# Performance work log

Hardware: AMD Instinct MI355X
Metric: run time of the kernel (lower is better)

Reference implementation:

```python
import jax, jax.numpy as jnp
import numpy as np

D_MODEL = 1024
NUM_HEADS = 16
D_K = D_MODEL // NUM_HEADS


def setup_inputs() -> dict:
    key = jax.random.key(0)
    ks = jax.random.split(key, 11)
    B, S = 4, 2048
    s = 1.0 / np.sqrt(D_MODEL)
    return {
        "q": jax.random.normal(ks[0], (B, S, D_MODEL), jnp.float32),
        "k": jax.random.normal(ks[1], (B, S, D_MODEL), jnp.float32),
        "v": jax.random.normal(ks[2], (B, S, D_MODEL), jnp.float32),
        "w_q": jax.random.normal(ks[3], (D_MODEL, D_MODEL), jnp.float32) * s,
        "b_q": jnp.zeros((D_MODEL,), jnp.float32),
        "w_k": jax.random.normal(ks[4], (D_MODEL, D_MODEL), jnp.float32) * s,
        "b_k": jnp.zeros((D_MODEL,), jnp.float32),
        "w_v": jax.random.normal(ks[5], (D_MODEL, D_MODEL), jnp.float32) * s,
        "b_v": jnp.zeros((D_MODEL,), jnp.float32),
        "w_o": jax.random.normal(ks[6], (D_MODEL, D_MODEL), jnp.float32) * s,
        "b_o": jnp.zeros((D_MODEL,), jnp.float32),
    }


def reference(q, k, v, w_q, b_q, w_k, b_k, w_v, b_v, w_o, b_o):
    B, S, _ = q.shape
    # projections; torch Linear computes x @ W.T + b
    def proj(x, w, b):
        y = x @ w.T + b
        return y.reshape(B, -1, NUM_HEADS, D_K).transpose(0, 2, 1, 3)  # (B,H,S,d_k)

    qh, kh, vh = proj(q, w_q, b_q), proj(k, w_k, b_k), proj(v, w_v, b_v)
    scores = jnp.einsum("bhqd,bhkd->bhqk", qh, kh) / jnp.sqrt(jnp.float32(D_K))
    attn_weights = jax.nn.softmax(scores, axis=-1)
    x = jnp.einsum("bhqk,bhkd->bhqd", attn_weights, vh)
    x = x.transpose(0, 2, 1, 3).reshape(B, -1, D_MODEL)
    out = x @ w_o.T + b_o
    return out, attn_weights
```

## Files before the change

### kernel.cpp

```cpp
#include <hip/hip_runtime.h>
#include <math.h>

#define S_LEN 2048
#define DM 1024
#define NH 16
#define DK 64

typedef __attribute__((ext_vector_type(8))) short short8;
typedef __attribute__((ext_vector_type(4))) short short4v;
typedef __attribute__((ext_vector_type(4))) float f32x4;

__device__ __forceinline__ short f2bf(float f) {
  unsigned u = __builtin_bit_cast(unsigned, f);
  u = (u + 0x7FFFu + ((u >> 16) & 1u)) >> 16;
  return (short)u;
}

__device__ __forceinline__ void gld_lds16(const short* g, short* l) {
  __builtin_amdgcn_global_load_lds(
      (const __attribute__((address_space(1))) unsigned int*)g,
      (__attribute__((address_space(3))) unsigned int*)l, 16, 0, 0);
}

__global__ __launch_bounds__(256) void cvt_bf16(
    const float* __restrict__ s0, const float* __restrict__ s1,
    const float* __restrict__ s2, const float* __restrict__ s3,
    short* __restrict__ d0, short* __restrict__ d1,
    short* __restrict__ d2, short* __restrict__ d3, int n)
{
  const float* s; short* d;
  switch (blockIdx.y) {
    case 0:  s = s0; d = d0; break;
    case 1:  s = s1; d = d1; break;
    case 2:  s = s2; d = d2; break;
    default: s = s3; d = d3; break;
  }
  const int i = (blockIdx.x * 256 + threadIdx.x) * 8;
  if (i < n) {
    const float4 v0 = *(const float4*)&s[i];
    const float4 v1 = *(const float4*)&s[i + 4];
    short8 r = { f2bf(v0.x), f2bf(v0.y), f2bf(v0.z), f2bf(v0.w),
                 f2bf(v1.x), f2bf(v1.y), f2bf(v1.z), f2bf(v1.w) };
    *(short8*)&d[i] = r;
  }
}

__global__ __launch_bounds__(256) void proj3(
    const short* __restrict__ qb, const short* __restrict__ kb, const short* __restrict__ vb,
    const short* __restrict__ wqb, const short* __restrict__ wkb, const short* __restrict__ wvb,
    const float* __restrict__ biq, const float* __restrict__ bik, const float* __restrict__ biv,
    short* __restrict__ qhb, short* __restrict__ khb, short* __restrict__ vtb)
{
  __shared__ short As[128 * 32];
  __shared__ short Bs[128 * 32];
  const int z = blockIdx.z;
  const short* A; const short* B; const float* bias; short* o;
  if (z == 0)      { A = qb; B = wqb; bias = biq; o = qhb; }
  else if (z == 1) { A = kb; B = wkb; bias = bik; o = khb; }
  else             { A = vb; B = wvb; bias = biv; o = vtb; }

  const int tid = threadIdx.x;
  const int lane = tid & 63;
  const int wv = tid >> 6;
  const int grp = lane >> 4, lid = lane & 15;
  const int wr = wv >> 1, wc = wv & 1;
  const int bm = blockIdx.x, bn = blockIdx.y;

  f32x4 acc[4][4] = {};

  const int idx0 = tid, idx1 = 256 + tid;
  const int r0 = idx0 >> 2, c0 = (idx0 & 3) * 8;
  const int r1 = idx1 >> 2, c1 = (idx1 & 3) * 8;
  const short* a0 = &A[(size_t)(bm * 128 + r0) * DM + c0];
  const short* a1 = &A[(size_t)(bm * 128 + r1) * DM + c1];
  const short* b0 = &B[(size_t)(bn * 128 + r0) * DM + c0];
  const short* b1 = &B[(size_t)(bn * 128 + r1) * DM + c1];

  for (int ks = 0; ks < 32; ++ks) {
    __syncthreads();
    gld_lds16(a0 + ks * 32, &As[idx0 * 8]);
    gld_lds16(a1 + ks * 32, &As[idx1 * 8]);
    gld_lds16(b0 + ks * 32, &Bs[idx0 * 8]);
    gld_lds16(b1 + ks * 32, &Bs[idx1 * 8]);
    __syncthreads();
    short8 a[4], b[4];
    #pragma unroll
    for (int m = 0; m < 4; ++m) a[m] = *(const short8*)&As[(wr * 64 + m * 16 + lid) * 32 + grp * 8];
    #pragma unroll
    for (int n = 0; n < 4; ++n) b[n] = *(const short8*)&Bs[(wc * 64 + n * 16 + lid) * 32 + grp * 8];
    #pragma unroll
    for (int m = 0; m < 4; ++m)
      #pragma unroll
      for (int n = 0; n < 4; ++n)
        acc[m][n] = __builtin_amdgcn_mfma_f32_16x16x32_bf16(a[m], b[n], acc[m][n], 0, 0, 0);
  }

  #pragma unroll
  for (int n = 0; n < 4; ++n) {
    const int ng = bn * 128 + wc * 64 + n * 16 + lid;
    const float bvs = bias[ng];
    const int h = ng >> 6, d = ng & 63;
    #pragma unroll
    for (int m = 0; m < 4; ++m) {
      const int mg = bm * 128 + wr * 64 + m * 16 + grp * 4;
      const int bb = mg >> 11, s = mg & 2047;
      if (z < 2) {
        #pragma unroll
        for (int r = 0; r < 4; ++r)
          o[(((size_t)bb * NH + h) * S_LEN + s + r) * DK + d] = f2bf(acc[m][n][r] + bvs);
      } else {
        short4v sv = { f2bf(acc[m][n][0] + bvs), f2bf(acc[m][n][1] + bvs),
                       f2bf(acc[m][n][2] + bvs), f2bf(acc[m][n][3] + bvs) };
        *(short4v*)&o[(((size_t)bb * NH + h) * DK + d) * S_LEN + s] = sv;
      }
    }
  }
}

__global__ __launch_bounds__(256) void gemm_o(
    const short* __restrict__ A, const short* __restrict__ B,
    const float* __restrict__ bias, float* __restrict__ of)
{
  __shared__ short As[128 * 32];
  __shared__ short Bs[128 * 32];
  const int tid = threadIdx.x;
  const int lane = tid & 63;
  const int wv = tid >> 6;
  const int grp = lane >> 4, lid = lane & 15;
  const int wr = wv >> 1, wc = wv & 1;
  const int bm = blockIdx.x, bn = blockIdx.y;

  f32x4 acc[4][4] = {};

  const int idx0 = tid, idx1 = 256 + tid;
  const int r0 = idx0 >> 2, c0 = (idx0 & 3) * 8;
  const int r1 = idx1 >> 2, c1 = (idx1 & 3) * 8;
  const short* a0 = &A[(size_t)(bm * 128 + r0) * DM + c0];
  const short* a1 = &A[(size_t)(bm * 128 + r1) * DM + c1];
  const short* b0 = &B[(size_t)(bn * 128 + r0) * DM + c0];
  const short* b1 = &B[(size_t)(bn * 128 + r1) * DM + c1];

  for (int ks = 0; ks < 32; ++ks) {
    __syncthreads();
    gld_lds16(a0 + ks * 32, &As[idx0 * 8]);
    gld_lds16(a1 + ks * 32, &As[idx1 * 8]);
    gld_lds16(b0 + ks * 32, &Bs[idx0 * 8]);
    gld_lds16(b1 + ks * 32, &Bs[idx1 * 8]);
    __syncthreads();
    short8 a[4], b[4];
    #pragma unroll
    for (int m = 0; m < 4; ++m) a[m] = *(const short8*)&As[(wr * 64 + m * 16 + lid) * 32 + grp * 8];
    #pragma unroll
    for (int n = 0; n < 4; ++n) b[n] = *(const short8*)&Bs[(wc * 64 + n * 16 + lid) * 32 + grp * 8];
    #pragma unroll
    for (int m = 0; m < 4; ++m)
      #pragma unroll
      for (int n = 0; n < 4; ++n)
        acc[m][n] = __builtin_amdgcn_mfma_f32_16x16x32_bf16(a[m], b[n], acc[m][n], 0, 0, 0);
  }

  #pragma unroll
  for (int n = 0; n < 4; ++n) {
    const int ng = bn * 128 + wc * 64 + n * 16 + lid;
    const float bvs = bias[ng];
    #pragma unroll
    for (int m = 0; m < 4; ++m) {
      const int mg = bm * 128 + wr * 64 + m * 16 + grp * 4;
      #pragma unroll
      for (int r = 0; r < 4; ++r)
        __builtin_nontemporal_store(acc[m][n][r] + bvs, &of[(size_t)(mg + r) * DM + ng]);
    }
  }
}

__global__ __launch_bounds__(128) void mha_attn6(
    const short* __restrict__ qh, const short* __restrict__ kh, const short* __restrict__ vt,
    float* __restrict__ attn, short* __restrict__ xb)
{
  __shared__ short Kt[64][72];
  __shared__ short Vt[64][72];
  __shared__ short Ps[2][32][72];

  const int tid = threadIdx.x;
  const int lane = tid & 63, wv = tid >> 6, grp = lane >> 4, lid = lane & 15;

  const int nid = blockIdx.x;
  const int x = nid & 7, jj = nid >> 3;
  const int bh = x + 8 * (jj >> 5);
  const int qt = jj & 31;

  const size_t baseQ = (size_t)bh * S_LEN * DK;
  const size_t baseV = (size_t)bh * DK * S_LEN;
  const float scale = 0.125f;

  const short* Qb = qh + baseQ;
  const short* Kb = kh + baseQ;
  const short* Vb = vt + baseV;

  int tr[4], tc[4];
  #pragma unroll
  for (int i = 0; i < 4; ++i) {
    const int id = tid + 128 * i;
    tr[i] = id >> 3; tc[i] = (id & 7) * 8;
  }

  short8 aq[2][2];
  #pragma unroll
  for (int mf = 0; mf < 2; ++mf)
    #pragma unroll
    for (int kf = 0; kf < 2; ++kf)
      aq[mf][kf] = *(const short8*)&Qb[(size_t)(qt * 64 + wv * 32 + mf * 16 + lid) * DK + kf * 32 + grp * 8];

  float lsum[2][4] = {};

  short8 kr[4];
  #pragma unroll
  for (int i = 0; i < 4; ++i) kr[i] = *(const short8*)&Kb[(size_t)tr[i] * DK + tc[i]];
  for (int kt = 0; kt < 32; ++kt) {
    short* buf = (kt & 1) ? &Ps[0][0][0] : &Kt[0][0];
    #pragma unroll
    for (int i = 0; i < 4; ++i) *(short8*)&buf[tr[i] * 72 + tc[i]] = kr[i];
    if (kt < 31) {
      #pragma unroll
      for (int i = 0; i < 4; ++i)
        kr[i] = *(const short8*)&Kb[(size_t)((kt + 1) * 64 + tr[i]) * DK + tc[i]];
    }
    __syncthreads();
    f32x4 sacc[2][4] = {};
    __builtin_amdgcn_s_setprio(1);
    #pragma unroll
    for (int kf = 0; kf < 2; ++kf) {
      short8 bk[4];
      #pragma unroll
      for (int nf = 0; nf < 4; ++nf) bk[nf] = *(const short8*)&buf[(nf * 16 + lid) * 72 + kf * 32 + grp * 8];
      #pragma unroll
      for (int mf = 0; mf < 2; ++mf)
        #pragma unroll
        for (int nf = 0; nf < 4; ++nf)
          sacc[mf][nf] = __builtin_amdgcn_mfma_f32_16x16x32_bf16(aq[mf][kf], bk[nf], sacc[mf][nf], 0, 0, 0);
    }
    __builtin_amdgcn_s_setprio(0);
    #pragma unroll
    for (int mf = 0; mf < 2; ++mf)
      #pragma unroll
      for (int r = 0; r < 4; ++r)
        #pragma unroll
        for (int nf = 0; nf < 4; ++nf)
          lsum[mf][r] += __expf(sacc[mf][nf][r] * scale);
  }

  float rl[2][4];
  #pragma unroll
  for (int mf = 0; mf < 2; ++mf)
    #pragma unroll
    for (int r = 0; r < 4; ++r) {
      float s = lsum[mf][r];
      #pragma unroll
      for (int off = 8; off >= 1; off >>= 1) s += __shfl_xor(s, off, 16);
      rl[mf][r] = 1.f / s;
    }

  f32x4 oacc[2][4] = {};
  float* attnB = attn + ((size_t)bh * S_LEN + qt * 64 + wv * 32) * S_LEN;

  short8 vr[4];
  #pragma unroll
  for (int i = 0; i < 4; ++i) {
    kr[i] = *(const short8*)&Kb[(size_t)tr[i] * DK + tc[i]];
    vr[i] = *(const short8*)&Vb[(size_t)tr[i] * S_LEN + tc[i]];
  }
  for (int kt = 0; kt < 32; ++kt) {
    __syncthreads();
    #pragma unroll
    for (int i = 0; i < 4; ++i) {
      *(short8*)&Kt[tr[i]][tc[i]] = kr[i];
      *(short8*)&Vt[tr[i]][tc[i]] = vr[i];
    }
    if (kt < 31) {
      #pragma unroll
      for (int i = 0; i < 4; ++i) {
        kr[i] = *(const short8*)&Kb[(size_t)((kt + 1) * 64 + tr[i]) * DK + tc[i]];
        vr[i] = *(const short8*)&Vb[(size_t)tr[i] * S_LEN + (kt + 1) * 64 + tc[i]];
      }
    }
    __syncthreads();

    f32x4 sacc[2][4] = {};
    __builtin_amdgcn_s_setprio(1);
    #pragma unroll
    for (int kf = 0; kf < 2; ++kf) {
      short8 bk[4];
      #pragma unroll
      for (int nf = 0; nf < 4; ++nf) bk[nf] = *(const short8*)&Kt[nf * 16 + lid][kf * 32 + grp * 8];
      #pragma unroll
      for (int mf = 0; mf < 2; ++mf)
        #pragma unroll
        for (int nf = 0; nf < 4; ++nf)
          sacc[mf][nf] = __builtin_amdgcn_mfma_f32_16x16x32_bf16(aq[mf][kf], bk[nf], sacc[mf][nf], 0, 0, 0);
    }
    __builtin_amdgcn_s_setprio(0);

    #pragma unroll
    for (int mf = 0; mf < 2; ++mf)
      #pragma unroll
      for (int nf = 0; nf < 4; ++nf)
        #pragma unroll
        for (int r = 0; r < 4; ++r) {
          const float p = __expf(sacc[mf][nf][r] * scale) * rl[mf][r];
          Ps[wv][mf * 16 + grp * 4 + r][nf * 16 + lid] = f2bf(p);
        }

    __builtin_amdgcn_s_setprio(1);
    #pragma unroll
    for (int kf = 0; kf < 2; ++kf) {
      short8 ap[2], bvv[4];
      #pragma unroll
      for (int mf = 0; mf < 2; ++mf) ap[mf] = *(const short8*)&Ps[wv][mf * 16 + lid][kf * 32 + grp * 8];
      #pragma unroll
      for (int nf = 0; nf < 4; ++nf) bvv[nf] = *(const short8*)&Vt[nf * 16 + lid][kf * 32 + grp * 8];
      #pragma unroll
      for (int mf = 0; mf < 2; ++mf)
        #pragma unroll
        for (int nf = 0; nf < 4; ++nf)
          oacc[mf][nf] = __builtin_amdgcn_mfma_f32_16x16x32_bf16(ap[mf], bvv[nf], oacc[mf][nf], 0, 0, 0);
    }
    __builtin_amdgcn_s_setprio(0);

    #pragma unroll
    for (int i = 0; i < 8; ++i) {
      const int qrow = i * 4 + grp;
      const uint2 u = *(const uint2*)&Ps[wv][qrow][lid * 4];
      f32x4 f;
      f[0] = __builtin_bit_cast(float, u.x << 16);
      f[1] = __builtin_bit_cast(float, u.x & 0xffff0000u);
      f[2] = __builtin_bit_cast(float, u.y << 16);
      f[3] = __builtin_bit_cast(float, u.y & 0xffff0000u);
      __builtin_nontemporal_store(f, (f32x4*)&attnB[(size_t)qrow * S_LEN + kt * 64 + lid * 4]);
    }
  }

  const int b = bh >> 4, h = bh & 15;
  #pragma unroll
  for (int mf = 0; mf < 2; ++mf) {
    #pragma unroll
    for (int nf = 0; nf < 4; ++nf) {
      #pragma unroll
      for (int r = 0; r < 4; ++r) {
        const int s = qt * 64 + wv * 32 + mf * 16 + grp * 4 + r;
        const int d = nf * 16 + lid;
        xb[((size_t)b * S_LEN + s) * DM + h * DK + d] = f2bf(oacc[mf][nf][r]);
      }
    }
  }
}

template<int MODE>
__global__ __launch_bounds__(256) void mha_gemm(
    const float* __restrict__ Af, const short* __restrict__ Ab,
    const float* __restrict__ W, const float* __restrict__ bias,
    short* __restrict__ obf, float* __restrict__ of)
{
  __shared__ short As[128][40];
  __shared__ short Bs[128][40];
  const int tid = threadIdx.x;
  const int lane = tid & 63, wv = tid >> 6;
  const int grp = lane >> 4, lid = lane & 15;
  const int wr = wv >> 1, wc = wv & 1;
  const int bm = blockIdx.x, bn = blockIdx.y;

  f32x4 acc[4][4] = {};

  for (int ks = 0; ks < 32; ++ks) {
    __syncthreads();
    if (MODE == 0) {
      #pragma unroll
      for (int i = 0; i < 4; ++i) {
        const int c = tid + 256 * i;
        const int row = c >> 3, kc = c & 7;
        const float4 v = *(const float4*)&Af[(size_t)(bm * 128 + row) * DM + ks * 32 + kc * 4];
        short4v s4 = { f2bf(v.x), f2bf(v.y), f2bf(v.z), f2bf(v.w) };
        *(short4v*)&As[row][kc * 4] = s4;
      }
    } else {
      #pragma unroll
      for (int i = 0; i < 2; ++i) {
        const int c = tid + 256 * i;
        const int row = c >> 2, k8 = (c & 3) * 8;
        *(float4*)&As[row][k8] = *(const float4*)&Ab[(size_t)(bm * 128 + row) * DM + ks * 32 + k8];
      }
    }
    #pragma unroll
    for (int i = 0; i < 4; ++i) {
      const int c = tid + 256 * i;
      const int row = c >> 3, kc = c & 7;
      const float4 v = *(const float4*)&W[(size_t)(bn * 128 + row) * DM + ks * 32 + kc * 4];
      short4v s4 = { f2bf(v.x), f2bf(v.y), f2bf(v.z), f2bf(v.w) };
      *(short4v*)&Bs[row][kc * 4] = s4;
    }
    __syncthreads();
    short8 a[4], b[4];
    #pragma unroll
    for (int m = 0; m < 4; ++m) a[m] = *(const short8*)&As[wr * 64 + m * 16 + lid][grp * 8];
    #pragma unroll
    for (int n = 0; n < 4; ++n) b[n] = *(const short8*)&Bs[wc * 64 + n * 16 + lid][grp * 8];
    #pragma unroll
    for (int m = 0; m < 4; ++m)
      #pragma unroll
      for (int n = 0; n < 4; ++n)
        acc[m][n] = __builtin_amdgcn_mfma_f32_16x16x32_bf16(a[m], b[n], acc[m][n], 0, 0, 0);
  }

  #pragma unroll
  for (int n = 0; n < 4; ++n) {
    const int ng = bn * 128 + wc * 64 + n * 16 + lid;
    const float bvs = bias[ng];
    #pragma unroll
    for (int m = 0; m < 4; ++m) {
      const int mg = bm * 128 + wr * 64 + m * 16 + grp * 4;
      #pragma unroll
      for (int r = 0; r < 4; ++r) {
        const float val = acc[m][n][r] + bvs;
        const int mm = mg + r;
        if (MODE == 0) {
          const int bb = mm >> 11, s = mm & 2047, h = ng >> 6, d = ng & 63;
          obf[(((size_t)bb * NH + h) * S_LEN + s) * DK + d] = f2bf(val);
        } else {
          of[(size_t)mm * DM + ng] = val;
        }
      }
    }
  }
}

__global__ __launch_bounds__(256) void mha_attn_old(
    const short* __restrict__ qh, const short* __restrict__ kh, const short* __restrict__ vh,
    float* __restrict__ attn, short* __restrict__ xb)
{
  __shared__ short QP[128][72];
  __shared__ short Ks[64][72];
  __shared__ short VT[64][72];

  const int tid = threadIdx.x;
  const int lane = tid & 63, wv = tid >> 6, grp = lane >> 4, lid = lane & 15;
  const int qt = blockIdx.x, bh = blockIdx.y;
  const size_t base = (size_t)bh * S_LEN * DK;
  const float scale = 0.125f;

  #pragma unroll
  for (int i = 0; i < 4; ++i) {
    const int c = tid + 256 * i;
    const int row = c >> 3, k8 = (c & 7) * 8;
    *(float4*)&QP[row][k8] = *(const float4*)&qh[base + (size_t)(qt * 128 + row) * DK + k8];
  }
  __syncthreads();
  short8 aq[2][2];
  #pragma unroll
  for (int mf = 0; mf < 2; ++mf)
    #pragma unroll
    for (int kf = 0; kf < 2; ++kf)
      aq[mf][kf] = *(const short8*)&QP[wv * 32 + mf * 16 + lid][kf * 32 + grp * 8];

  float lsum[2][4] = {};

  for (int kt = 0; kt < 32; ++kt) {
    __syncthreads();
    #pragma unroll
    for (int i = 0; i < 2; ++i) {
      const int c = tid + 256 * i;
      const int row = c >> 3, k8 = (c & 7) * 8;
      *(float4*)&Ks[row][k8] = *(const float4*)&kh[base + (size_t)(kt * 64 + row) * DK + k8];
    }
    __syncthreads();
    f32x4 sacc[2][4] = {};
    #pragma unroll
    for (int kf = 0; kf < 2; ++kf) {
      short8 bk[4];
      #pragma unroll
      for (int nf = 0; nf < 4; ++nf) bk[nf] = *(const short8*)&Ks[nf * 16 + lid][kf * 32 + grp * 8];
      #pragma unroll
      for (int mf = 0; mf < 2; ++mf)
        #pragma unroll
        for (int nf = 0; nf < 4; ++nf)
          sacc[mf][nf] = __builtin_amdgcn_mfma_f32_16x16x32_bf16(aq[mf][kf], bk[nf], sacc[mf][nf], 0, 0, 0);
    }
    #pragma unroll
    for (int mf = 0; mf < 2; ++mf)
      #pragma unroll
      for (int r = 0; r < 4; ++r)
        #pragma unroll
        for (int nf = 0; nf < 4; ++nf)
          lsum[mf][r] += __expf(sacc[mf][nf][r] * scale);
  }

  float rl[2][4];
  #pragma unroll
  for (int mf = 0; mf < 2; ++mf)
    #pragma unroll
    for (int r = 0; r < 4; ++r) {
      float s = lsum[mf][r];
      #pragma unroll
      for (int off = 8; off >= 1; off >>= 1) s += __shfl_xor(s, off, 16);
      rl[mf][r] = 1.f / s;
    }

  f32x4 oacc[2][4] = {};

  for (int kt = 0; kt < 32; ++kt) {
    __syncthreads();
    #pragma unroll
    for (int i = 0; i < 2; ++i) {
      const int c = tid + 256 * i;
      const int row = c >> 3, k8 = (c & 7) * 8;
      *(float4*)&Ks[row][k8] = *(const float4*)&kh[base + (size_t)(kt * 64 + row) * DK + k8];
    }
    #pragma unroll
    for (int i = 0; i < 2; ++i) {
      const int key = tid & 63;
      const int d0 = ((tid >> 6) << 3) + i * 32;
      const float4 v = *(const float4*)&vh[base + (size_t)(kt * 64 + key) * DK + d0];
      const short8 sv = __builtin_bit_cast(short8, v);
      #pragma unroll
      for (int jj = 0; jj < 8; ++jj) VT[d0 + jj][key] = sv[jj];
    }
    __syncthreads();
    f32x4 sacc[2][4] = {};
    #pragma unroll
    for (int kf = 0; kf < 2; ++kf) {
      short8 bk[4];
      #pragma unroll
      for (int nf = 0; nf < 4; ++nf) bk[nf] = *(const short8*)&Ks[nf * 16 + lid][kf * 32 + grp * 8];
      #pragma unroll
      for (int mf = 0; mf < 2; ++mf)
        #pragma unroll
        for (int nf = 0; nf < 4; ++nf)
          sacc[mf][nf] = __builtin_amdgcn_mfma_f32_16x16x32_bf16(aq[mf][kf], bk[nf], sacc[mf][nf], 0, 0, 0);
    }
    #pragma unroll
    for (int mf = 0; mf < 2; ++mf) {
      #pragma unroll
      for (int nf = 0; nf < 4; ++nf) {
        #pragma unroll
        for (int r = 0; r < 4; ++r) {
          const float p = __expf(sacc[mf][nf][r] * scale) * rl[mf][r];
          const int qr = wv * 32 + mf * 16 + grp * 4 + r;
          const int kc = kt * 64 + nf * 16 + lid;
          attn[((size_t)bh * S_LEN + qt * 128 + qr) * S_LEN + kc] = p;
          QP[wv * 32 + (qr & 31)][nf * 16 + lid] = f2bf(p);
        }
      }
    }
    #pragma unroll
    for (int kf = 0; kf < 2; ++kf) {
      short8 ap[2], bvv[4];
      #pragma unroll
      for (int mf = 0; mf < 2; ++mf) ap[mf] = *(const short8*)&QP[wv * 32 + mf * 16 + lid][kf * 32 + grp * 8];
      #pragma unroll
      for (int nf = 0; nf < 4; ++nf) bvv[nf] = *(const short8*)&VT[nf * 16 + lid][kf * 32 + grp * 8];
      #pragma unroll
      for (int mf = 0; mf < 2; ++mf)
        #pragma unroll
        for (int nf = 0; nf < 4; ++nf)
          oacc[mf][nf] = __builtin_amdgcn_mfma_f32_16x16x32_bf16(ap[mf], bvv[nf], oacc[mf][nf], 0, 0, 0);
    }
  }

  const int b = bh >> 4, h = bh & 15;
  #pragma unroll
  for (int mf = 0; mf < 2; ++mf) {
    #pragma unroll
    for (int nf = 0; nf < 4; ++nf) {
      #pragma unroll
      for (int r = 0; r < 4; ++r) {
        const int s = qt * 128 + wv * 32 + mf * 16 + grp * 4 + r;
        const int d = nf * 16 + lid;
        xb[((size_t)b * S_LEN + s) * DM + h * DK + d] = f2bf(oacc[mf][nf][r]);
      }
    }
  }
}

extern "C" void kernel_launch(void* const* d_in, const int* in_sizes, int n_in,
                              void* d_out, int out_size, void* d_ws, size_t ws_size,
                              hipStream_t stream) {
  const float* q  = (const float*)d_in[0];
  const float* k  = (const float*)d_in[1];
  const float* v  = (const float*)d_in[2];
  const float* wq = (const float*)d_in[3];
  const float* bq = (const float*)d_in[4];
  const float* wk = (const float*)d_in[5];
  const float* bk = (const float*)d_in[6];
  const float* wv = (const float*)d_in[7];
  const float* bv = (const float*)d_in[8];
  const float* wo = (const float*)d_in[9];
  const float* bo = (const float*)d_in[10];

  float* out  = (float*)d_out;
  float* attn = out + (size_t)4 * S_LEN * DM;

  const size_t NTOK = (size_t)4 * S_LEN * DM;
  const size_t NW   = (size_t)DM * DM;
  dim3 blk(256);

  if (ws_size >= 135000000ull) {
    short* qb  = (short*)d_ws;
    short* kb  = qb + NTOK;
    short* vb  = kb + NTOK;
    short* wqb = vb + NTOK;
    short* wkb = wqb + NW;
    short* wvb = wkb + NW;
    short* wob = wvb + NW;
    short* qhb = wob + NW;
    short* khb = qhb + NTOK;
    short* vtb = khb + NTOK;
    short* xb  = vtb + NTOK;

    cvt_bf16<<<dim3(4096, 3), blk, 0, stream>>>(q, k, v, (const float*)nullptr,
                                                qb, kb, vb, (short*)nullptr, (int)NTOK);
    cvt_bf16<<<dim3(512, 4), blk, 0, stream>>>(wq, wk, wv, wo, wqb, wkb, wvb, wob, (int)NW);

    proj3<<<dim3(64, 8, 3), blk, 0, stream>>>(qb, kb, vb, wqb, wkb, wvb, bq, bk, bv,
                                              qhb, khb, vtb);

    mha_attn6<<<dim3(2048), dim3(128), 0, stream>>>(qhb, khb, vtb, attn, xb);

    gemm_o<<<dim3(64, 8), blk, 0, stream>>>(xb, wob, bo, out);
  } else {
    short* qhb = (short*)d_ws;
    short* khb = qhb + NTOK;
    short* vhb = khb + NTOK;
    short* xb  = vhb + NTOK;

    mha_gemm<0><<<dim3(64, 8), blk, 0, stream>>>(q, (const short*)nullptr, wq, bq, qhb, (float*)nullptr);
    mha_gemm<0><<<dim3(64, 8), blk, 0, stream>>>(k, (const short*)nullptr, wk, bk, khb, (float*)nullptr);
    mha_gemm<0><<<dim3(64, 8), blk, 0, stream>>>(v, (const short*)nullptr, wv, bv, vhb, (float*)nullptr);
    mha_attn_old<<<dim3(16, 64), blk, 0, stream>>>(qhb, khb, vhb, attn, xb);
    mha_gemm<1><<<dim3(64, 8), blk, 0, stream>>>((const float*)nullptr, xb, wo, bo, (short*)nullptr, out);
  }
}
```

Baseline: 397.2 us.

## Transpose score MFMA operands and stage V-projection transpose through LDS

The attention kernel now computes S^T tiles by swapping the MFMA operands (K as A, Q as B). Each lane then holds four consecutive key columns for one query row, so the P tile is written to LDS as packed 4-short stores and the row-sum reduction needs only two cross-lane shuffles. Normalization folds into the exponent as exp(s*scale - log l) through an FMA, replacing the multiply by a reciprocal. Separately, the V projection writes its transposed output through a padded LDS tile so global stores become coalesced 16-byte rows, at the cost of a larger shared-memory footprint and extra barriers.

```diff
diff --git a/kernel.cpp b/kernel.cpp
--- a/kernel.cpp
+++ b/kernel.cpp
@@ -51,8 +51,10 @@
     const float* __restrict__ biq, const float* __restrict__ bik, const float* __restrict__ biv,
     short* __restrict__ qhb, short* __restrict__ khb, short* __restrict__ vtb)
 {
-  __shared__ short As[128 * 32];
-  __shared__ short Bs[128 * 32];
+  __shared__ short SM[17408];
+  short* As = SM;
+  short* Bs = SM + 4096;
+
   const int z = blockIdx.z;
   const short* A; const short* B; const float* bias; short* o;
   if (z == 0)      { A = qb; B = wqb; bias = biq; o = qhb; }
@@ -95,24 +97,44 @@
         acc[m][n] = __builtin_amdgcn_mfma_f32_16x16x32_bf16(a[m], b[n], acc[m][n], 0, 0, 0);
   }
 
-  #pragma unroll
-  for (int n = 0; n < 4; ++n) {
-    const int ng = bn * 128 + wc * 64 + n * 16 + lid;
-    const float bvs = bias[ng];
-    const int h = ng >> 6, d = ng & 63;
-    #pragma unroll
-    for (int m = 0; m < 4; ++m) {
-      const int mg = bm * 128 + wr * 64 + m * 16 + grp * 4;
-      const int bb = mg >> 11, s = mg & 2047;
-      if (z < 2) {
+  if (z < 2) {
+    #pragma unroll
+    for (int n = 0; n < 4; ++n) {
+      const int ng = bn * 128 + wc * 64 + n * 16 + lid;
+      const float bvs = bias[ng];
+      const int h = ng >> 6, d = ng & 63;
+      #pragma unroll
+      for (int m = 0; m < 4; ++m) {
+        const int mg = bm * 128 + wr * 64 + m * 16 + grp * 4;
+        const int bb = mg >> 11, s = mg & 2047;
         #pragma unroll
         for (int r = 0; r < 4; ++r)
           o[(((size_t)bb * NH + h) * S_LEN + s + r) * DK + d] = f2bf(acc[m][n][r] + bvs);
-      } else {
-        short4v sv = { f2bf(acc[m][n][0] + bvs), f2bf(acc[m][n][1] + bvs),
+      }
+    }
+  } else {
+    __syncthreads();
+    #pragma unroll
+    for (int n = 0; n < 4; ++n) {
+      const int ngl = wc * 64 + n * 16 + lid;
+      const float bvs = bias[bn * 128 + ngl];
+      #pragma unroll
+      for (int m = 0; m < 4; ++m) {
+        const int sl = wr * 64 + m * 16 + grp * 4;
+        short4v c4 = { f2bf(acc[m][n][0] + bvs), f2bf(acc[m][n][1] + bvs),
                        f2bf(acc[m][n][2] + bvs), f2bf(acc[m][n][3] + bvs) };
-        *(short4v*)&o[(((size_t)bb * NH + h) * DK + d) * S_LEN + s] = sv;
-      }
+        *(short4v*)&SM[ngl * 136 + sl] = c4;
+      }
+    }
+    __syncthreads();
+    const int bb = bm >> 4, s0 = (bm & 15) * 128;
+    #pragma unroll
+    for (int i = 0; i < 8; ++i) {
+      const int id = tid + 256 * i;
+      const int row = id >> 4;
+      const int c8 = (id & 15) * 8;
+      const short8 vv = *(const short8*)&SM[row * 136 + c8];
+      *(short8*)&o[((size_t)bb * 1024 + bn * 128 + row) * S_LEN + s0 + c8] = vv;
     }
   }
 }
@@ -173,7 +195,7 @@
   }
 }
 
-__global__ __launch_bounds__(128) void mha_attn6(
+__global__ __launch_bounds__(128) void mha_attn7(
     const short* __restrict__ qh, const short* __restrict__ kh, const short* __restrict__ vt,
     float* __restrict__ attn, short* __restrict__ xb)
 {
@@ -206,12 +228,12 @@
 
   short8 aq[2][2];
   #pragma unroll
-  for (int mf = 0; mf < 2; ++mf)
+  for (int qb2 = 0; qb2 < 2; ++qb2)
     #pragma unroll
     for (int kf = 0; kf < 2; ++kf)
-      aq[mf][kf] = *(const short8*)&Qb[(size_t)(qt * 64 + wv * 32 + mf * 16 + lid) * DK + kf * 32 + grp * 8];
-
-  float lsum[2][4] = {};
+      aq[qb2][kf] = *(const short8*)&Qb[(size_t)(qt * 64 + wv * 32 + qb2 * 16 + lid) * DK + kf * 32 + grp * 8];
+
+  float lsum[2] = {};
 
   short8 kr[4];
   #pragma unroll
@@ -226,39 +248,37 @@
         kr[i] = *(const short8*)&Kb[(size_t)((kt + 1) * 64 + tr[i]) * DK + tc[i]];
     }
     __syncthreads();
-    f32x4 sacc[2][4] = {};
+    f32x4 sacc[4][2] = {};
     __builtin_amdgcn_s_setprio(1);
     #pragma unroll
     for (int kf = 0; kf < 2; ++kf) {
-      short8 bk[4];
-      #pragma unroll
-      for (int nf = 0; nf < 4; ++nf) bk[nf] = *(const short8*)&buf[(nf * 16 + lid) * 72 + kf * 32 + grp * 8];
-      #pragma unroll
-      for (int mf = 0; mf < 2; ++mf)
-        #pragma unroll
-        for (int nf = 0; nf < 4; ++nf)
-          sacc[mf][nf] = __builtin_amdgcn_mfma_f32_16x16x32_bf16(aq[mf][kf], bk[nf], sacc[mf][nf], 0, 0, 0);
+      short8 ak[4];
+      #pragma unroll
+      for (int kb2 = 0; kb2 < 4; ++kb2) ak[kb2] = *(const short8*)&buf[(kb2 * 16 + lid) * 72 + kf * 32 + grp * 8];
+      #pragma unroll
+      for (int kb2 = 0; kb2 < 4; ++kb2)
+        #pragma unroll
+        for (int qb2 = 0; qb2 < 2; ++qb2)
+          sacc[kb2][qb2] = __builtin_amdgcn_mfma_f32_16x16x32_bf16(ak[kb2], aq[qb2][kf], sacc[kb2][qb2], 0, 0, 0);
     }
     __builtin_amdgcn_s_setprio(0);
     #pragma unroll
-    for (int mf = 0; mf < 2; ++mf)
-      #pragma unroll
-      for (int r = 0; r < 4; ++r)
-        #pragma unroll
-        for (int nf = 0; nf < 4; ++nf)
-          lsum[mf][r] += __expf(sacc[mf][nf][r] * scale);
-  }
-
-  float rl[2][4];
-  #pragma unroll
-  for (int mf = 0; mf < 2; ++mf)
-    #pragma unroll
-    for (int r = 0; r < 4; ++r) {
-      float s = lsum[mf][r];
-      #pragma unroll
-      for (int off = 8; off >= 1; off >>= 1) s += __shfl_xor(s, off, 16);
-      rl[mf][r] = 1.f / s;
-    }
+    for (int qb2 = 0; qb2 < 2; ++qb2)
+      #pragma unroll
+      for (int kb2 = 0; kb2 < 4; ++kb2)
+        #pragma unroll
+        for (int r = 0; r < 4; ++r)
+          lsum[qb2] += __expf(sacc[kb2][qb2][r] * scale);
+  }
+
+  float logl[2];
+  #pragma unroll
+  for (int qb2 = 0; qb2 < 2; ++qb2) {
+    float s = lsum[qb2];
+    s += __shfl_xor(s, 16);
+    s += __shfl_xor(s, 32);
+    logl[qb2] = __logf(s);
+  }
 
   f32x4 oacc[2][4] = {};
   float* attnB = attn + ((size_t)bh * S_LEN + qt * 64 + wv * 32) * S_LEN;
@@ -285,30 +305,33 @@
     }
     __syncthreads();
 
-    f32x4 sacc[2][4] = {};
+    f32x4 sacc[4][2] = {};
     __builtin_amdgcn_s_setprio(1);
     #pragma unroll
     for (int kf = 0; kf < 2; ++kf) {
-      short8 bk[4];
-      #pragma unroll
-      for (int nf = 0; nf < 4; ++nf) bk[nf] = *(const short8*)&Kt[nf * 16 + lid][kf * 32 + grp * 8];
-      #pragma unroll
-      for (int mf = 0; mf < 2; ++mf)
-        #pragma unroll
-        for (int nf = 0; nf < 4; ++nf)
-          sacc[mf][nf] = __builtin_amdgcn_mfma_f32_16x16x32_bf16(aq[mf][kf], bk[nf], sacc[mf][nf], 0, 0, 0);
+      short8 ak[4];
+      #pragma unroll
+      for (int kb2 = 0; kb2 < 4; ++kb2) ak[kb2] = *(const short8*)&Kt[kb2 * 16 + lid][kf * 32 + grp * 8];
+      #pragma unroll
+      for (int kb2 = 0; kb2 < 4; ++kb2)
+        #pragma unroll
+        for (int qb2 = 0; qb2 < 2; ++qb2)
+          sacc[kb2][qb2] = __builtin_amdgcn_mfma_f32_16x16x32_bf16(ak[kb2], aq[qb2][kf], sacc[kb2][qb2], 0, 0, 0);
     }
     __builtin_amdgcn_s_setprio(0);
 
     #pragma unroll
-    for (int mf = 0; mf < 2; ++mf)
-      #pragma unroll
-      for (int nf = 0; nf < 4; ++nf)
-        #pragma unroll
-        for (int r = 0; r < 4; ++r) {
-          const float p = __expf(sacc[mf][nf][r] * scale) * rl[mf][r];
-          Ps[wv][mf * 16 + grp * 4 + r][nf * 16 + lid] = f2bf(p);
-        }
+    for (int qb2 = 0; qb2 < 2; ++qb2) {
+      const float nl = -logl[qb2];
+      #pragma unroll
+      for (int kb2 = 0; kb2 < 4; ++kb2) {
+        short4v p4;
+        #pragma unroll
+        for (int r = 0; r < 4; ++r)
+          p4[r] = f2bf(__expf(__builtin_fmaf(sacc[kb2][qb2][r], scale, nl)));
+        *(short4v*)&Ps[wv][qb2 * 16 + lid][kb2 * 16 + grp * 4] = p4;
+      }
+    }
 
     __builtin_amdgcn_s_setprio(1);
     #pragma unroll
@@ -621,7 +644,7 @@
     proj3<<<dim3(64, 8, 3), blk, 0, stream>>>(qb, kb, vb, wqb, wkb, wvb, bq, bk, bv,
                                               qhb, khb, vtb);
 
-    mha_attn6<<<dim3(2048), dim3(128), 0, stream>>>(qhb, khb, vtb, attn, xb);
+    mha_attn7<<<dim3(2048), dim3(128), 0, stream>>>(qhb, khb, vtb, attn, xb);
 
     gemm_o<<<dim3(64, 8), blk, 0, stream>>>(xb, wob, bo, out);
   } else {
```

Result: faster. 386.9 us (-2.6%).
